# Kernel optimization log

Hardware: AMD Instinct MI355X
Metric: run time of the kernel (lower is better)

The kernel has to match this reference:

```python
import jax, jax.numpy as jnp
import numpy as np

DIMS, HEAD, FREQ = 1024, 16, 10000
HEAD_DIM = DIMS // HEAD          # 64
ROT = HEAD_DIM // 2              # 32
B, S = 4, 8192


def setup_inputs() -> dict:
    key = jax.random.key(0)
    k1, k2, k3, k4 = jax.random.split(key, 4)
    x = jax.random.normal(k1, (B, S, DIMS), dtype=jnp.float32)
    matrix = jax.random.normal(k2, (HEAD_DIM, HEAD_DIM), dtype=jnp.float32)
    thetas = jax.random.normal(k3, (ROT,), dtype=jnp.float32) * 0.1
    tscale = jnp.ones((1,), dtype=jnp.float32)
    # inverse frequencies exactly as in __init__
    invf = (1.0 / FREQ ** (jnp.arange(0, HEAD_DIM, 2, dtype=jnp.float32) / HEAD_DIM)).astype(jnp.float32)
    pairs = jax.random.randint(k4, (ROT, 2), 0, HEAD_DIM, dtype=jnp.int32)
    return {"x": x, "matrix": matrix, "thetas": thetas, "tscale": tscale,
            "invf": invf, "pairs": pairs}


def _composed_rotation(thetas, tscale, pairs, d, dtype):
    # Build every Givens matrix G_k (same element-set order as the torch code)
    theta = thetas * tscale[0]

    def make_G(i, j, th):
        c, sn = jnp.cos(th), jnp.sin(th)
        G = jnp.eye(d, dtype=dtype)
        return G.at[i, i].set(c).at[j, j].set(c).at[i, j].set(-sn).at[j, i].set(sn)

    Gs = jax.vmap(make_G)(pairs[:, 0], pairs[:, 1], theta)  # [rot, d, d]

    def step(acc, G):
        return acc @ G, None

    G_comb, _ = jax.lax.scan(step, jnp.eye(d, dtype=dtype), Gs)
    return G_comb


def reference(x, matrix, thetas, tscale, invf, pairs):
    b, s, dims = x.shape
    d = matrix.shape[0]          # head_dim
    h = dims // d                # heads

    G_comb = _composed_rotation(thetas, tscale, pairs, d, x.dtype)

    xr = x.reshape(b, s, h, d)
    # flat @ G_combined @ self.matrix (acts on last dim)
    xr = xr @ (G_comb @ matrix)

    # sinusoidal RoPE: sinusoid[s, d/2] = pos * invf
    pos = jnp.arange(s, dtype=x.dtype)
    sinusoid = pos[:, None] * invf[None, :]
    sin = jnp.sin(sinusoid)[None, :, None, :]   # [1, s, 1, d/2]
    cos = jnp.cos(sinusoid)[None, :, None, :]

    x1, x2 = xr[..., ::2], xr[..., 1::2]
    out = jnp.concatenate([x1 * cos - x2 * sin, x1 * sin + x2 * cos], axis=-1)
    return out.reshape(b, s, dims) * jnp.asarray(np.sqrt(dims), x.dtype)
```

## Files before the change

### kernel.cpp

```cpp
#include <hip/hip_runtime.h>
#include <math.h>

#define BB 4
#define SS 8192
#define HH 16
#define DD 64
#define ROT 32
#define NG (BB * SS * HH)
#define RPB 64
#define LSTR 65
#define TPB 256

typedef float f32x4 __attribute__((ext_vector_type(4)));

__global__ void setup_GM(const float* __restrict__ thetas,
                         const float* __restrict__ tscale,
                         const int* __restrict__ pairs,
                         const float* __restrict__ matrix,
                         float* __restrict__ M) {
  __shared__ float Gs[DD][DD];
  const int t = threadIdx.x;
  if (t < DD) {
    for (int c = 0; c < DD; ++c) Gs[t][c] = (t == c) ? 1.0f : 0.0f;
    const float ts = tscale[0];
    for (int r = 0; r < ROT; ++r) {
      const int i = pairs[2 * r], j = pairs[2 * r + 1];
      const float th = thetas[r] * ts;
      const float cc = cosf(th), sn = sinf(th);
      if (i == j) {
        Gs[t][i] *= sn;
      } else {
        const float a = Gs[t][i], b = Gs[t][j];
        Gs[t][i] = a * cc + b * sn;
        Gs[t][j] = b * cc - a * sn;
      }
    }
  }
  __syncthreads();
  const int e = blockIdx.x * 256 + t;
  const int row = e >> 6, col = e & 63;
  float a0 = 0.f, a1 = 0.f, a2 = 0.f, a3 = 0.f;
  for (int k = 0; k < DD; k += 4) {
    a0 = fmaf(Gs[row][k], matrix[k * DD + col], a0);
    a1 = fmaf(Gs[row][k + 1], matrix[(k + 1) * DD + col], a1);
    a2 = fmaf(Gs[row][k + 2], matrix[(k + 2) * DD + col], a2);
    a3 = fmaf(Gs[row][k + 3], matrix[(k + 3) * DD + col], a3);
  }
  M[e] = (a0 + a1) + (a2 + a3);
}

__global__ void setup_table(const float* __restrict__ invf,
                            float* __restrict__ tab) {
  const int idx = blockIdx.x * 256 + threadIdx.x;
  if (idx >= SS * 32) return;
  const int s = idx >> 5, d = idx & 31;
  const float ang = (float)s * invf[d];
  tab[s * 64 + d] = 32.0f * cosf(ang);
  tab[s * 64 + 32 + d] = 32.0f * sinf(ang);
}

__global__ __launch_bounds__(TPB, 8) void apply_rot(
    const float* __restrict__ x, const float* __restrict__ M,
    const float* __restrict__ tab, const float* __restrict__ invf,
    float* __restrict__ out) {
  __shared__ float lds[RPB * LSTR];
  const int tid = threadIdx.x;
  const size_t R0 = (size_t)blockIdx.x * RPB;

  const float4* __restrict__ xg = (const float4*)x + R0 * 16;
#pragma unroll
  for (int i = 0; i < 4; ++i) {
    const int f = i * TPB + tid;
    const int row = f >> 4, c4 = f & 15;
    const float4 v = xg[f];
    *(float4*)&lds[row * LSTR + c4 * 4] = v;
  }
  __syncthreads();

  const int r = tid & (RPB - 1);
  const int h = __builtin_amdgcn_readfirstlane(tid >> 6);
  const float* __restrict__ Mh = M + h * 16;
  const float* __restrict__ xr = &lds[r * LSTR];

  float acc[16];
#pragma unroll
  for (int c = 0; c < 16; ++c) acc[c] = 0.0f;

#pragma unroll 4
  for (int k4 = 0; k4 < 16; ++k4) {
    const float4 xv = *(const float4*)&xr[k4 * 4];
    const float* __restrict__ m0 = Mh + k4 * 4 * DD;
#pragma unroll
    for (int c = 0; c < 16; ++c) acc[c] = fmaf(xv.x, m0[c], acc[c]);
#pragma unroll
    for (int c = 0; c < 16; ++c) acc[c] = fmaf(xv.y, m0[DD + c], acc[c]);
#pragma unroll
    for (int c = 0; c < 16; ++c) acc[c] = fmaf(xv.z, m0[2 * DD + c], acc[c]);
#pragma unroll
    for (int c = 0; c < 16; ++c) acc[c] = fmaf(xv.w, m0[3 * DD + c], acc[c]);
  }

  const int g = (int)R0 + r;
  const int spos = (g >> 4) & (SS - 1);
  float cz[8], sz[8];
  if (tab) {
    const float4* __restrict__ tc = (const float4*)(tab + spos * 64 + h * 8);
    const float4* __restrict__ tn =
        (const float4*)(tab + spos * 64 + 32 + h * 8);
    *(float4*)&cz[0] = tc[0];
    *(float4*)&cz[4] = tc[1];
    *(float4*)&sz[0] = tn[0];
    *(float4*)&sz[4] = tn[1];
  } else {
#pragma unroll
    for (int d = 0; d < 8; ++d) {
      const float ang = (float)spos * invf[h * 8 + d];
      cz[d] = 32.0f * cosf(ang);
      sz[d] = 32.0f * sinf(ang);
    }
  }

  float4 lov[2], hiv[2];
#pragma unroll
  for (int q = 0; q < 2; ++q) {
#pragma unroll
    for (int d = 0; d < 4; ++d) {
      const int dd = 4 * q + d;
      const float e = acc[2 * dd], o = acc[2 * dd + 1];
      ((float*)&lov[q])[d] = e * cz[dd] - o * sz[dd];
      ((float*)&hiv[q])[d] = e * sz[dd] + o * cz[dd];
    }
  }

  __syncthreads();
  float* __restrict__ orow = &lds[r * LSTR];
  *(float4*)&orow[8 * h + 0] = lov[0];
  *(float4*)&orow[8 * h + 4] = lov[1];
  *(float4*)&orow[32 + 8 * h + 0] = hiv[0];
  *(float4*)&orow[32 + 8 * h + 4] = hiv[1];
  __syncthreads();

  float4* __restrict__ og = (float4*)out + R0 * 16;
#pragma unroll
  for (int i = 0; i < 4; ++i) {
    const int f = i * TPB + tid;
    const float4 v = *(const float4*)&lds[(f >> 4) * LSTR + (f & 15) * 4];
    __builtin_nontemporal_store(*(const f32x4*)&v, (f32x4*)&og[f]);
  }
}

extern "C" void kernel_launch(void* const* d_in, const int* in_sizes, int n_in,
                              void* d_out, int out_size, void* d_ws,
                              size_t ws_size, hipStream_t stream) {
  const float* x = (const float*)d_in[0];
  const float* matrix = (const float*)d_in[1];
  const float* thetas = (const float*)d_in[2];
  const float* tscale = (const float*)d_in[3];
  const float* invf = (const float*)d_in[4];
  const int* pairs = (const int*)d_in[5];
  float* out = (float*)d_out;

  float* M = (float*)d_ws;
  float* tab = M + DD * DD;
  const size_t need = (size_t)(DD * DD + SS * 64) * sizeof(float);
  const bool have_tab = ws_size >= need;

  setup_GM<<<16, 256, 0, stream>>>(thetas, tscale, pairs, matrix, M);
  if (have_tab) setup_table<<<(SS * 32) / 256, 256, 0, stream>>>(invf, tab);
  apply_rot<<<NG / RPB, TPB, 0, stream>>>(x, M, have_tab ? tab : nullptr, invf,
                                          out);
}
```

Measured before the change: 279.1 us.

## Compute per-head projection with split-bf16 MFMA and multi-tile blocks

Replaces the scalar FMA matrix multiply with bf16 MFMA instructions. Both x and the combined matrix are split into hi and lo bf16 parts, and three products (hh, hl, lh) are summed to approximate fp32 accuracy. The matrix fragments are pre-swizzled in setup and stay in registers. Each block processes four tiles of 64 rows, prefetching the next tile's x directly into registers, and the RoPE pairing is done with lane shuffles and an LDS transpose for coalesced stores. The goal is to make the kernel memory bound rather than ALU bound, at the cost of slightly reduced precision and lower occupancy.

Result: faster. 263.2 us (-5.7%).

```diff
diff --git a/kernel.cpp b/kernel.cpp
--- a/kernel.cpp
+++ b/kernel.cpp
@@ -7,17 +7,23 @@
 #define DD 64
 #define ROT 32
 #define NG (BB * SS * HH)
-#define RPB 64
+#define RPT 64
+#define TILES 4
+#define NBLK (NG / (RPT * TILES))
+#define TPB 256
+#define OSTR 65
 #define LSTR 65
-#define TPB 256
 
 typedef float f32x4 __attribute__((ext_vector_type(4)));
+typedef short bf16x8 __attribute__((ext_vector_type(8)));
 
 __global__ void setup_GM(const float* __restrict__ thetas,
                          const float* __restrict__ tscale,
                          const int* __restrict__ pairs,
                          const float* __restrict__ matrix,
-                         float* __restrict__ M) {
+                         float* __restrict__ M,
+                         unsigned short* __restrict__ Mhi,
+                         unsigned short* __restrict__ Mlo) {
   __shared__ float Gs[DD][DD];
   const int t = threadIdx.x;
   if (t < DD) {
@@ -38,15 +44,25 @@
   }
   __syncthreads();
   const int e = blockIdx.x * 256 + t;
-  const int row = e >> 6, col = e & 63;
+  const int k = e >> 6, col = e & 63;
   float a0 = 0.f, a1 = 0.f, a2 = 0.f, a3 = 0.f;
-  for (int k = 0; k < DD; k += 4) {
-    a0 = fmaf(Gs[row][k], matrix[k * DD + col], a0);
-    a1 = fmaf(Gs[row][k + 1], matrix[(k + 1) * DD + col], a1);
-    a2 = fmaf(Gs[row][k + 2], matrix[(k + 2) * DD + col], a2);
-    a3 = fmaf(Gs[row][k + 3], matrix[(k + 3) * DD + col], a3);
-  }
-  M[e] = (a0 + a1) + (a2 + a3);
+  for (int kk = 0; kk < DD; kk += 4) {
+    a0 = fmaf(Gs[k][kk], matrix[kk * DD + col], a0);
+    a1 = fmaf(Gs[k][kk + 1], matrix[(kk + 1) * DD + col], a1);
+    a2 = fmaf(Gs[k][kk + 2], matrix[(kk + 2) * DD + col], a2);
+    a3 = fmaf(Gs[k][kk + 3], matrix[(kk + 3) * DD + col], a3);
+  }
+  const float val = (a0 + a1) + (a2 + a3);
+  M[e] = val;
+
+  const int K2 = k >> 5, T = col >> 4;
+  const int lane = ((k >> 3) & 3) * 16 + (col & 15);
+  const int idx = ((T * 2 + K2) * 64 + lane) * 8 + (k & 7);
+  const unsigned int b = __float_as_uint(val);
+  const unsigned int hb = b & 0xFFFF0000u;
+  const float rem = val - __uint_as_float(hb);
+  Mhi[idx] = (unsigned short)(b >> 16);
+  Mlo[idx] = (unsigned short)(__float_as_uint(rem) >> 16);
 }
 
 __global__ void setup_table(const float* __restrict__ invf,
@@ -59,33 +75,136 @@
   tab[s * 64 + 32 + d] = 32.0f * sinf(ang);
 }
 
-__global__ __launch_bounds__(TPB, 8) void apply_rot(
+__device__ __forceinline__ unsigned int pack_hi(float u, float v, float& ru,
+                                                float& rv) {
+  const unsigned int bu = __float_as_uint(u);
+  const unsigned int bv = __float_as_uint(v);
+  const unsigned int hv = bv & 0xFFFF0000u;
+  ru = u - __uint_as_float(bu & 0xFFFF0000u);
+  rv = v - __uint_as_float(hv);
+  return (bu >> 16) | hv;
+}
+__device__ __forceinline__ unsigned int pack_lo(float ru, float rv) {
+  return (__float_as_uint(ru) >> 16) | (__float_as_uint(rv) & 0xFFFF0000u);
+}
+__device__ __forceinline__ void cvt8(const f32x4 a, const f32x4 b, bf16x8& hi,
+                                     bf16x8& lo) {
+  unsigned int* hp = (unsigned int*)&hi;
+  unsigned int* lp = (unsigned int*)&lo;
+  float r0, r1;
+  hp[0] = pack_hi(a[0], a[1], r0, r1);
+  lp[0] = pack_lo(r0, r1);
+  hp[1] = pack_hi(a[2], a[3], r0, r1);
+  lp[1] = pack_lo(r0, r1);
+  hp[2] = pack_hi(b[0], b[1], r0, r1);
+  lp[2] = pack_lo(r0, r1);
+  hp[3] = pack_hi(b[2], b[3], r0, r1);
+  lp[3] = pack_lo(r0, r1);
+}
+
+__global__ __launch_bounds__(TPB, 2) void apply_rot(
+    const float* __restrict__ x, const unsigned short* __restrict__ Mhi,
+    const unsigned short* __restrict__ Mlo, const float* __restrict__ tab,
+    float* __restrict__ out) {
+  __shared__ float po[4 * 16 * OSTR];
+  const int tid = threadIdx.x;
+  const int w = tid >> 6;
+  const int l = tid & 63;
+  const int l15 = l & 15, lk = l >> 4;
+  const int odd = l & 1;
+  const int dloc = l15 >> 1;
+
+  bf16x8 bh[8], bl[8];
+#pragma unroll
+  for (int f = 0; f < 8; ++f) {
+    bh[f] = *(const bf16x8*)(Mhi + (f * 64 + l) * 8);
+    bl[f] = *(const bf16x8*)(Mlo + (f * 64 + l) * 8);
+  }
+
+  const size_t R0 = (size_t)blockIdx.x * (RPT * TILES);
+  const float* __restrict__ xp = x + (R0 + w * 16 + l15) * DD + lk * 8;
+  float* __restrict__ pw = po + w * 16 * OSTR;
+
+  f32x4 x0 = *(const f32x4*)(xp);
+  f32x4 x1 = *(const f32x4*)(xp + 4);
+  f32x4 x2 = *(const f32x4*)(xp + 32);
+  f32x4 x3 = *(const f32x4*)(xp + 36);
+
+#pragma unroll 1
+  for (int t = 0; t < TILES; ++t) {
+    bf16x8 ah0, al0, ah1, al1;
+    cvt8(x0, x1, ah0, al0);
+    cvt8(x2, x3, ah1, al1);
+
+    if (t + 1 < TILES) {
+      xp += RPT * DD;
+      x0 = *(const f32x4*)(xp);
+      x1 = *(const f32x4*)(xp + 4);
+      x2 = *(const f32x4*)(xp + 32);
+      x3 = *(const f32x4*)(xp + 36);
+    }
+
+    f32x4 acc[4];
+#pragma unroll
+    for (int T = 0; T < 4; ++T) {
+      f32x4 a = {0.f, 0.f, 0.f, 0.f};
+      a = __builtin_amdgcn_mfma_f32_16x16x32_bf16(ah0, bh[T * 2 + 0], a, 0, 0, 0);
+      a = __builtin_amdgcn_mfma_f32_16x16x32_bf16(ah1, bh[T * 2 + 1], a, 0, 0, 0);
+      a = __builtin_amdgcn_mfma_f32_16x16x32_bf16(ah0, bl[T * 2 + 0], a, 0, 0, 0);
+      a = __builtin_amdgcn_mfma_f32_16x16x32_bf16(ah1, bl[T * 2 + 1], a, 0, 0, 0);
+      a = __builtin_amdgcn_mfma_f32_16x16x32_bf16(al0, bh[T * 2 + 0], a, 0, 0, 0);
+      a = __builtin_amdgcn_mfma_f32_16x16x32_bf16(al1, bh[T * 2 + 1], a, 0, 0, 0);
+      acc[T] = a;
+    }
+
+    const int spos = (int)((R0 >> 4) + t * 4 + w) & (SS - 1);
+    const float* __restrict__ tb = tab + spos * 64;
+#pragma unroll
+    for (int T = 0; T < 4; ++T) {
+      const float cz = tb[8 * T + dloc];
+      const float sz = tb[32 + 8 * T + dloc];
+      const int ocol = (odd ? 32 : 0) + 8 * T + dloc;
+#pragma unroll
+      for (int q = 0; q < 4; ++q) {
+        const float v = acc[T][q];
+        const float p = __shfl_xor(v, 1);
+        const float ps = p * sz;
+        const float res = fmaf(v, cz, odd ? ps : -ps);
+        pw[(lk * 4 + q) * OSTR + ocol] = res;
+      }
+    }
+
+    float* __restrict__ og = out + (R0 + (size_t)t * RPT + w * 16) * DD;
+#pragma unroll
+    for (int jj = 0; jj < 4; ++jj) {
+      const int f = jj * 64 + l;
+      const int row = f >> 4, c4 = (f & 15) * 4;
+      const f32x4 v = *(const f32x4*)&pw[row * OSTR + c4];
+      __builtin_nontemporal_store(v, (f32x4*)(og + row * DD + c4));
+    }
+  }
+}
+
+__global__ __launch_bounds__(256, 8) void apply_rot_fb(
     const float* __restrict__ x, const float* __restrict__ M,
-    const float* __restrict__ tab, const float* __restrict__ invf,
-    float* __restrict__ out) {
-  __shared__ float lds[RPB * LSTR];
+    const float* __restrict__ invf, float* __restrict__ out) {
+  __shared__ float lds[64 * LSTR];
   const int tid = threadIdx.x;
-  const size_t R0 = (size_t)blockIdx.x * RPB;
-
+  const size_t R0 = (size_t)blockIdx.x * 64;
   const float4* __restrict__ xg = (const float4*)x + R0 * 16;
 #pragma unroll
   for (int i = 0; i < 4; ++i) {
-    const int f = i * TPB + tid;
-    const int row = f >> 4, c4 = f & 15;
-    const float4 v = xg[f];
-    *(float4*)&lds[row * LSTR + c4 * 4] = v;
-  }
-  __syncthreads();
-
-  const int r = tid & (RPB - 1);
+    const int f = i * 256 + tid;
+    *(float4*)&lds[(f >> 4) * LSTR + (f & 15) * 4] = xg[f];
+  }
+  __syncthreads();
+  const int r = tid & 63;
   const int h = __builtin_amdgcn_readfirstlane(tid >> 6);
   const float* __restrict__ Mh = M + h * 16;
   const float* __restrict__ xr = &lds[r * LSTR];
-
   float acc[16];
 #pragma unroll
   for (int c = 0; c < 16; ++c) acc[c] = 0.0f;
-
 #pragma unroll 4
   for (int k4 = 0; k4 < 16; ++k4) {
     const float4 xv = *(const float4*)&xr[k4 * 4];
@@ -99,27 +218,15 @@
 #pragma unroll
     for (int c = 0; c < 16; ++c) acc[c] = fmaf(xv.w, m0[3 * DD + c], acc[c]);
   }
-
   const int g = (int)R0 + r;
   const int spos = (g >> 4) & (SS - 1);
   float cz[8], sz[8];
-  if (tab) {
-    const float4* __restrict__ tc = (const float4*)(tab + spos * 64 + h * 8);
-    const float4* __restrict__ tn =
-        (const float4*)(tab + spos * 64 + 32 + h * 8);
-    *(float4*)&cz[0] = tc[0];
-    *(float4*)&cz[4] = tc[1];
-    *(float4*)&sz[0] = tn[0];
-    *(float4*)&sz[4] = tn[1];
-  } else {
-#pragma unroll
-    for (int d = 0; d < 8; ++d) {
-      const float ang = (float)spos * invf[h * 8 + d];
-      cz[d] = 32.0f * cosf(ang);
-      sz[d] = 32.0f * sinf(ang);
-    }
-  }
-
+#pragma unroll
+  for (int d = 0; d < 8; ++d) {
+    const float ang = (float)spos * invf[h * 8 + d];
+    cz[d] = 32.0f * cosf(ang);
+    sz[d] = 32.0f * sinf(ang);
+  }
   float4 lov[2], hiv[2];
 #pragma unroll
   for (int q = 0; q < 2; ++q) {
@@ -131,7 +238,6 @@
       ((float*)&hiv[q])[d] = e * sz[dd] + o * cz[dd];
     }
   }
-
   __syncthreads();
   float* __restrict__ orow = &lds[r * LSTR];
   *(float4*)&orow[8 * h + 0] = lov[0];
@@ -139,13 +245,11 @@
   *(float4*)&orow[32 + 8 * h + 0] = hiv[0];
   *(float4*)&orow[32 + 8 * h + 4] = hiv[1];
   __syncthreads();
-
   float4* __restrict__ og = (float4*)out + R0 * 16;
 #pragma unroll
   for (int i = 0; i < 4; ++i) {
-    const int f = i * TPB + tid;
-    const float4 v = *(const float4*)&lds[(f >> 4) * LSTR + (f & 15) * 4];
-    __builtin_nontemporal_store(*(const f32x4*)&v, (f32x4*)&og[f]);
+    const int f = i * 256 + tid;
+    og[f] = *(float4*)&lds[(f >> 4) * LSTR + (f & 15) * 4];
   }
 }
 
@@ -161,12 +265,18 @@
   float* out = (float*)d_out;
 
   float* M = (float*)d_ws;
-  float* tab = M + DD * DD;
-  const size_t need = (size_t)(DD * DD + SS * 64) * sizeof(float);
+  unsigned short* Mhi = (unsigned short*)(M + DD * DD);
+  unsigned short* Mlo = Mhi + DD * DD;
+  float* tab = (float*)(Mlo + DD * DD);
+  const size_t need =
+      (size_t)DD * DD * 4 + (size_t)DD * DD * 4 + (size_t)SS * 64 * 4;
   const bool have_tab = ws_size >= need;
 
-  setup_GM<<<16, 256, 0, stream>>>(thetas, tscale, pairs, matrix, M);
-  if (have_tab) setup_table<<<(SS * 32) / 256, 256, 0, stream>>>(invf, tab);
-  apply_rot<<<NG / RPB, TPB, 0, stream>>>(x, M, have_tab ? tab : nullptr, invf,
-                                          out);
-}
+  setup_GM<<<16, 256, 0, stream>>>(thetas, tscale, pairs, matrix, M, Mhi, Mlo);
+  if (have_tab) {
+    setup_table<<<(SS * 32) / 256, 256, 0, stream>>>(invf, tab);
+    apply_rot<<<NBLK, TPB, 0, stream>>>(x, Mhi, Mlo, tab, out);
+  } else {
+    apply_rot_fb<<<NG / 64, 256, 0, stream>>>(x, M, invf, out);
+  }
+}
```
